# Kernel tuning notes

Hardware: AMD Instinct MI355X
Metric: run time of the kernel (lower is better)

## Reference

```python
import jax, jax.numpy as jnp
import numpy as np

N, E, IN, HID, OUT = 100000, 1600000, 128, 128, 64


def setup_inputs() -> dict:
    key = jax.random.key(0)
    ks = jax.random.split(key, 8)
    x = jax.random.normal(ks[0], (N, IN), dtype=jnp.float32)
    edge_index = jax.random.randint(ks[1], (2, E), 0, N, dtype=jnp.int64)
    s = lambda fan_in: 1.0 / np.sqrt(fan_in)
    W1_l = jax.random.normal(ks[2], (IN, HID), dtype=jnp.float32) * s(IN)
    W1_r = jax.random.normal(ks[3], (IN, HID), dtype=jnp.float32) * s(IN)
    b1 = jnp.zeros((HID,), dtype=jnp.float32)
    W2_l = jax.random.normal(ks[4], (HID, OUT), dtype=jnp.float32) * s(HID)
    W2_r = jax.random.normal(ks[5], (HID, OUT), dtype=jnp.float32) * s(HID)
    b2 = jnp.zeros((OUT,), dtype=jnp.float32)
    return {"x": x, "edge_index": edge_index, "W1_l": W1_l, "W1_r": W1_r,
            "b1": b1, "W2_l": W2_l, "W2_r": W2_r, "b2": b2}


def sage_conv(x, src, dst, W_l, W_r, b):
    """PyG SAGEConv (aggr='mean', root_weight=True): lin_l(mean_agg) + lin_r(x)."""
    n = x.shape[0]
    msg = x[src]                                              # [E, d] gather
    agg = jax.ops.segment_sum(msg, dst, num_segments=n)       # [N, d] scatter-add
    deg = jax.ops.segment_sum(jnp.ones_like(dst, dtype=x.dtype), dst,
                              num_segments=n)                 # [N]
    mean = agg / jnp.maximum(deg, 1.0)[:, None]
    return mean @ W_l + x @ W_r + b


def reference(x, edge_index, W1_l, W1_r, b1, W2_l, W2_r, b2):
    src, dst = edge_index[0], edge_index[1]
    h = sage_conv(x, src, dst, W1_l, W1_r, b1)
    h = jax.nn.relu(h)
    # dropout(p=0.5) is identity in eval mode
    out = sage_conv(h, src, dst, W2_l, W2_r, b2)
    return out
```

## Files before the change

kernel.cpp:

```cpp
#include <hip/hip_runtime.h>

#define NN 100000
#define NE 1600000
#define PSHIFT 9
#define PSZ 512
#define NP ((NN + PSZ - 1) / PSZ)
#define BCHUNK 8192
#define NBIN ((NE + BCHUNK - 1) / BCHUNK)
#define SRCMASK 0x1FFFF
#define BUCKET 9216
#define GMTILES ((NN + 63) / 64)
#define GEMM_GB 512

typedef __attribute__((ext_vector_type(8))) short short8;
typedef __attribute__((ext_vector_type(4))) float f32x4;

__device__ __forceinline__ ushort f2bf(float f) {
    uint u = __float_as_uint(f);
    return (ushort)((u + 0x7FFFu + ((u >> 16) & 1u)) >> 16);
}
__device__ __forceinline__ float bflo(uint u) { return __uint_as_float(u << 16); }
__device__ __forceinline__ float bfhi(uint u) { return __uint_as_float(u & 0xffff0000u); }
__device__ __forceinline__ uint packbf(float a, float b) {
    return (uint)f2bf(a) | ((uint)f2bf(b) << 16);
}

__global__ __launch_bounds__(256) void k_prep(const float* __restrict__ W1l,
                                              const float* __restrict__ W1r,
                                              const float* __restrict__ W2l,
                                              const float* __restrict__ W2r,
                                              ushort* __restrict__ WbT1,
                                              ushort* __restrict__ WbT2,
                                              int* __restrict__ gcur)
{
    const int tid = threadIdx.x;
    if (blockIdx.x == 0) {
        if (tid < NP) gcur[tid] = tid * BUCKET;
        return;
    }
    int i = (blockIdx.x - 1) * 256 + tid;
    if (i < 256 * 128) {
        int c = i >> 7, k = i & 127;
        float v = (c < 128) ? W1l[k * 128 + c] : W1r[k * 128 + (c - 128)];
        WbT1[i] = f2bf(v);
    } else if (i < 256 * 128 + 128 * 128) {
        int j = i - 256 * 128;
        int c = j >> 7, k = j & 127;
        float v = (c < 64) ? W2l[k * 64 + c] : W2r[k * 64 + (c - 64)];
        WbT2[j] = f2bf(v);
    }
}

__global__ __launch_bounds__(256) void k_binning(const int* __restrict__ src,
                                                 const int* __restrict__ dst,
                                                 int* __restrict__ gcur,
                                                 uint* __restrict__ packed)
{
    __shared__ int cnt[256];
    __shared__ int base[256];
    const int tid = threadIdx.x;
    const long e0 = (long)blockIdx.x * BCHUNK;
    cnt[tid] = 0;
    __syncthreads();
    for (int i = tid; i < BCHUNK; i += 256) {
        long e = e0 + i;
        if (e < NE) atomicAdd(&cnt[dst[e] >> PSHIFT], 1);
    }
    __syncthreads();
    if (cnt[tid] > 0) base[tid] = atomicAdd(&gcur[tid], cnt[tid]);
    cnt[tid] = 0;
    __syncthreads();
    for (int i = tid; i < BCHUNK; i += 256) {
        long e = e0 + i;
        if (e < NE) {
            int d = dst[e], s = src[e];
            int p = d >> PSHIFT;
            int ofs = atomicAdd(&cnt[p], 1);
            packed[base[p] + ofs] = (uint)s | ((uint)(d & (PSZ - 1)) << 17);
        }
    }
}

__global__ __launch_bounds__(256) void k_pfill(const uint* __restrict__ packed,
                                               const int* __restrict__ gcur,
                                               int* __restrict__ rowptr,
                                               int* __restrict__ rowend,
                                               int* __restrict__ col)
{
    __shared__ int cnt[PSZ];
    __shared__ int cur[PSZ];
    __shared__ int tot[256];
    const int p   = blockIdx.x;
    const int tid = threadIdx.x;
    const int beg = p * BUCKET, end = gcur[p];
    cnt[tid] = 0; cnt[tid + 256] = 0;
    __syncthreads();
    for (int i = beg + tid; i < end; i += 256)
        atomicAdd(&cnt[packed[i] >> 17], 1);
    __syncthreads();
    int v0 = cnt[tid * 2], v1 = cnt[tid * 2 + 1];
    int s  = v0 + v1;
    tot[tid] = s;
    __syncthreads();
    for (int off = 1; off < 256; off <<= 1) {
        int t = (tid >= off) ? tot[tid - off] : 0;
        __syncthreads();
        tot[tid] += t;
        __syncthreads();
    }
    int ex = tot[tid] - s + beg;
    cur[tid * 2]     = ex;
    cur[tid * 2 + 1] = ex + v0;
    int n0 = p * PSZ;
    if (n0 + tid * 2 < NN) {
        rowptr[n0 + tid * 2] = ex;
        rowend[n0 + tid * 2] = ex + v0;
    }
    if (n0 + tid * 2 + 1 < NN) {
        rowptr[n0 + tid * 2 + 1] = ex + v0;
        rowend[n0 + tid * 2 + 1] = ex + v0 + v1;
    }
    __syncthreads();
    for (int i = beg + tid; i < end; i += 256) {
        uint v = packed[i];
        int pos = atomicAdd(&cur[v >> 17], 1);
        col[pos] = (int)(v & SRCMASK);
    }
}

template <bool AF32, int CB, bool YF32>
__global__ __launch_bounds__(512) void k_gemm(const void* __restrict__ Ap,
                                              const ushort* __restrict__ Bt,
                                              const float* __restrict__ bias,
                                              ushort* __restrict__ zb,
                                              void* __restrict__ yout)
{
    constexpr int ZW = CB * 64;
    __shared__ ushort As[2][64 * 128];

    const int tid  = threadIdx.x;
    const int wid  = tid >> 6, lane = tid & 63;
    const int lr   = lane & 15;
    const int lk   = (lane >> 4) << 3;

    short8 bfr[4][CB];
#pragma unroll
    for (int ks = 0; ks < 4; ++ks)
#pragma unroll
        for (int nf = 0; nf < CB; ++nf) {
            int colB = wid * (16 * CB) + nf * 16 + lr;
            bfr[ks][nf] = *reinterpret_cast<const short8*>(
                Bt + (size_t)colB * 128 + ks * 32 + lk);
        }

    const int p0 = tid * 16, p1 = p0 + 8192;
    const int r0 = p0 >> 8, r1 = p1 >> 8;
    const int d0 = p0 ^ ((r0 & 7) << 4);
    const int d1 = p1 ^ ((r1 & 7) << 4);
    const int e0 = (p0 & 255) >> 1;
    const int e1 = (p1 & 255) >> 1;

    const short8 zero8 = {0, 0, 0, 0, 0, 0, 0, 0};
    short8 sA0, sA1;

    auto loadA = [&](int gr, int eo) -> short8 {
        if (gr >= NN) return zero8;
        if (AF32) {
            const float* A = (const float*)Ap;
            float4 f0 = *reinterpret_cast<const float4*>(A + (size_t)gr * 128 + eo);
            float4 f1 = *reinterpret_cast<const float4*>(A + (size_t)gr * 128 + eo + 4);
            short8 v;
            v[0] = (short)f2bf(f0.x); v[1] = (short)f2bf(f0.y);
            v[2] = (short)f2bf(f0.z); v[3] = (short)f2bf(f0.w);
            v[4] = (short)f2bf(f1.x); v[5] = (short)f2bf(f1.y);
            v[6] = (short)f2bf(f1.z); v[7] = (short)f2bf(f1.w);
            return v;
        } else {
            const ushort* A = (const ushort*)Ap;
            return *reinterpret_cast<const short8*>(A + (size_t)gr * 128 + eo);
        }
    };

    int t = blockIdx.x;
    sA0 = loadA(t * 64 + r0, e0);
    sA1 = loadA(t * 64 + r1, e1);

    int cur = 0;
    for (; t < GMTILES; t += GEMM_GB) {
        char* wbase = reinterpret_cast<char*>(As[cur]);
        *reinterpret_cast<short8*>(wbase + d0) = sA0;
        *reinterpret_cast<short8*>(wbase + d1) = sA1;
        __syncthreads();

        int tn = t + GEMM_GB;
        if (tn < GMTILES) {
            sA0 = loadA(tn * 64 + r0, e0);
            sA1 = loadA(tn * 64 + r1, e1);
        }

        f32x4 acc[4][CB];
#pragma unroll
        for (int mi = 0; mi < 4; ++mi)
#pragma unroll
            for (int nf = 0; nf < CB; ++nf) acc[mi][nf] = f32x4{0.f, 0.f, 0.f, 0.f};

        const char* pA = reinterpret_cast<const char*>(As[cur]);
#pragma unroll
        for (int ks = 0; ks < 4; ++ks) {
            int k2 = (ks * 32 + lk) * 2;
            short8 a[4];
#pragma unroll
            for (int mi = 0; mi < 4; ++mi) {
                int r = mi * 16 + lr;
                int byte = (r * 256 + k2) ^ ((r & 7) << 4);
                a[mi] = *reinterpret_cast<const short8*>(pA + byte);
            }
#pragma unroll
            for (int mi = 0; mi < 4; ++mi)
#pragma unroll
                for (int nf = 0; nf < CB; ++nf)
                    acc[mi][nf] = __builtin_amdgcn_mfma_f32_16x16x32_bf16(
                        a[mi], bfr[ks][nf], acc[mi][nf], 0, 0, 0);
        }

#pragma unroll
        for (int mi = 0; mi < 4; ++mi) {
#pragma unroll
            for (int nf = 0; nf < CB; ++nf) {
                int colg = wid * (16 * CB) + nf * 16 + lr;
#pragma unroll
                for (int rr = 0; rr < 4; ++rr) {
                    int rowg = t * 64 + mi * 16 + ((lane >> 4) << 2) + rr;
                    if (rowg < NN) {
                        float v = acc[mi][nf][rr];
                        if (colg < ZW) {
                            zb[(size_t)rowg * ZW + colg] = f2bf(v);
                        } else {
                            int c2 = colg - ZW;
                            if (YF32) ((float*)yout)[(size_t)rowg * ZW + c2]  = v + bias[c2];
                            else      ((ushort*)yout)[(size_t)rowg * ZW + c2] = f2bf(v + bias[c2]);
                        }
                    }
                }
            }
        }
        cur ^= 1;
    }
}

__global__ __launch_bounds__(256) void k_gather1(const ushort* __restrict__ z1b,
                                                 const ushort* __restrict__ y1b,
                                                 const int* __restrict__ rowptr,
                                                 const int* __restrict__ rowend,
                                                 const int* __restrict__ col,
                                                 ushort* __restrict__ hb)
{
    const int w = threadIdx.x >> 6, lane = threadIdx.x & 63;
    const int n = blockIdx.x * 4 + w;
    if (n >= NN) return;
    const int half = lane >> 5, li = lane & 31;
    const int beg = rowptr[n], end = rowend[n];
    const uint2* zu = (const uint2*)z1b;
    float a0 = 0.f, a1 = 0.f, a2 = 0.f, a3 = 0.f;
    int e = beg;
    for (; e + 7 < end; e += 8) {
        int s0 = col[e     + half];
        int s1 = col[e + 2 + half];
        int s2 = col[e + 4 + half];
        int s3 = col[e + 6 + half];
        uint2 u0 = zu[(size_t)s0 * 32 + li];
        uint2 u1 = zu[(size_t)s1 * 32 + li];
        uint2 u2 = zu[(size_t)s2 * 32 + li];
        uint2 u3 = zu[(size_t)s3 * 32 + li];
        a0 += bflo(u0.x) + bflo(u1.x) + bflo(u2.x) + bflo(u3.x);
        a1 += bfhi(u0.x) + bfhi(u1.x) + bfhi(u2.x) + bfhi(u3.x);
        a2 += bflo(u0.y) + bflo(u1.y) + bflo(u2.y) + bflo(u3.y);
        a3 += bfhi(u0.y) + bfhi(u1.y) + bfhi(u2.y) + bfhi(u3.y);
    }
    for (; e + 1 < end; e += 2) {
        int s0 = col[e + half];
        uint2 u0 = zu[(size_t)s0 * 32 + li];
        a0 += bflo(u0.x); a1 += bfhi(u0.x);
        a2 += bflo(u0.y); a3 += bfhi(u0.y);
    }
    if (e < end && half == 0) {
        int s0 = col[e];
        uint2 u0 = zu[(size_t)s0 * 32 + li];
        a0 += bflo(u0.x); a1 += bfhi(u0.x);
        a2 += bflo(u0.y); a3 += bfhi(u0.y);
    }
    a0 += __shfl_xor(a0, 32); a1 += __shfl_xor(a1, 32);
    a2 += __shfl_xor(a2, 32); a3 += __shfl_xor(a3, 32);
    if (half == 0) {
        float inv = 1.0f / (float)max(end - beg, 1);
        uint2 uy = ((const uint2*)y1b)[(size_t)n * 32 + li];
        float h0 = fmaxf(a0 * inv + bflo(uy.x), 0.f);
        float h1 = fmaxf(a1 * inv + bfhi(uy.x), 0.f);
        float h2 = fmaxf(a2 * inv + bflo(uy.y), 0.f);
        float h3 = fmaxf(a3 * inv + bfhi(uy.y), 0.f);
        uint2 o;
        o.x = packbf(h0, h1);
        o.y = packbf(h2, h3);
        ((uint2*)hb)[(size_t)n * 32 + li] = o;
    }
}

__global__ __launch_bounds__(256) void k_gather2(const ushort* __restrict__ z2b,
                                                 const float* __restrict__ y2f,
                                                 const int* __restrict__ rowptr,
                                                 const int* __restrict__ rowend,
                                                 const int* __restrict__ col,
                                                 float* __restrict__ out)
{
    const int w = threadIdx.x >> 6, lane = threadIdx.x & 63;
    const int n = blockIdx.x * 4 + w;
    if (n >= NN) return;
    const int quar = lane >> 4, li = lane & 15;
    const int beg = rowptr[n], end = rowend[n];
    const uint2* zu = (const uint2*)z2b;
    float a0 = 0.f, a1 = 0.f, a2 = 0.f, a3 = 0.f;
    int e = beg;
    for (; e + 15 < end; e += 16) {
        int s0 = col[e      + quar];
        int s1 = col[e + 4  + quar];
        int s2 = col[e + 8  + quar];
        int s3 = col[e + 12 + quar];
        uint2 u0 = zu[(size_t)s0 * 16 + li];
        uint2 u1 = zu[(size_t)s1 * 16 + li];
        uint2 u2 = zu[(size_t)s2 * 16 + li];
        uint2 u3 = zu[(size_t)s3 * 16 + li];
        a0 += bflo(u0.x) + bflo(u1.x) + bflo(u2.x) + bflo(u3.x);
        a1 += bfhi(u0.x) + bfhi(u1.x) + bfhi(u2.x) + bfhi(u3.x);
        a2 += bflo(u0.y) + bflo(u1.y) + bflo(u2.y) + bflo(u3.y);
        a3 += bfhi(u0.y) + bfhi(u1.y) + bfhi(u2.y) + bfhi(u3.y);
    }
    for (; e + 3 < end; e += 4) {
        int s0 = col[e + quar];
        uint2 u0 = zu[(size_t)s0 * 16 + li];
        a0 += bflo(u0.x); a1 += bfhi(u0.x);
        a2 += bflo(u0.y); a3 += bfhi(u0.y);
    }
    int rem = end - e;
    if (quar < rem) {
        int s0 = col[e + quar];
        uint2 u0 = zu[(size_t)s0 * 16 + li];
        a0 += bflo(u0.x); a1 += bfhi(u0.x);
        a2 += bflo(u0.y); a3 += bfhi(u0.y);
    }
    a0 += __shfl_xor(a0, 16); a1 += __shfl_xor(a1, 16);
    a2 += __shfl_xor(a2, 16); a3 += __shfl_xor(a3, 16);
    a0 += __shfl_xor(a0, 32); a1 += __shfl_xor(a1, 32);
    a2 += __shfl_xor(a2, 32); a3 += __shfl_xor(a3, 32);
    if (quar == 0) {
        float inv = 1.0f / (float)max(end - beg, 1);
        float4 y = ((const float4*)y2f)[(size_t)n * 16 + li];
        float4 o;
        o.x = a0 * inv + y.x;
        o.y = a1 * inv + y.y;
        o.z = a2 * inv + y.z;
        o.w = a3 * inv + y.w;
        ((float4*)out)[(size_t)n * 16 + li] = o;
    }
}

extern "C" void kernel_launch(void* const* d_in, const int* in_sizes, int n_in,
                              void* d_out, int out_size, void* d_ws, size_t ws_size,
                              hipStream_t stream)
{
    const float* x   = (const float*)d_in[0];
    const int*   ei  = (const int*)d_in[1];
    const float* W1l = (const float*)d_in[2];
    const float* W1r = (const float*)d_in[3];
    const float* b1  = (const float*)d_in[4];
    const float* W2l = (const float*)d_in[5];
    const float* W2r = (const float*)d_in[6];
    const float* b2  = (const float*)d_in[7];
    float* out = (float*)d_out;

    const int* src = ei;
    const int* dst = ei + NE;

    int*  rowptr = (int*)d_ws;
    int*  rowend = rowptr + NN;
    int*  gcur   = rowend + NN;
    uint* packed = (uint*)(gcur + 256);
    int*  colA   = (int*)(packed + (size_t)NP * BUCKET);
    uintptr_t p = (uintptr_t)(colA + (size_t)NP * BUCKET);
    p = (p + 255) & ~(uintptr_t)255;
    ushort* WbT1 = (ushort*)p;  p += (size_t)256 * 128 * 2;
    ushort* WbT2 = (ushort*)p;  p += (size_t)128 * 128 * 2;
    p = (p + 255) & ~(uintptr_t)255;
    ushort* z1b = (ushort*)p;   p += (size_t)NN * 128 * 2;
    ushort* y1b = (ushort*)p;   p += (size_t)NN * 128 * 2;
    ushort* hb  = (ushort*)p;   p += (size_t)NN * 128 * 2;
    ushort* z2b = z1b;
    float*  y2f = (float*)y1b;

    k_prep<<<1 + (256 * 128 + 128 * 128 + 255) / 256, 256, 0, stream>>>(
        W1l, W1r, W2l, W2r, WbT1, WbT2, gcur);

    k_binning<<<NBIN, 256, 0, stream>>>(src, dst, gcur, packed);
    k_pfill<<<NP, 256, 0, stream>>>(packed, gcur, rowptr, rowend, colA);

    k_gemm<true, 2, false><<<GEMM_GB, 512, 0, stream>>>(x, WbT1, b1, z1b, y1b);
    k_gather1<<<(NN + 3) / 4, 256, 0, stream>>>(z1b, y1b, rowptr, rowend, colA, hb);

    k_gemm<false, 1, true><<<GEMM_GB, 512, 0, stream>>>(hb, WbT2, b2, z2b, y2f);
    k_gather2<<<(NN + 3) / 4, 256, 0, stream>>>(z2b, y2f, rowptr, rowend, colA, out);
}
```

Baseline: 240.0 us.

## Slice feature columns per XCC and gather slices via persistent work-stealing blocks

```diff
diff --git a/kernel.cpp b/kernel.cpp
--- a/kernel.cpp
+++ b/kernel.cpp
@@ -11,6 +11,8 @@
 #define BUCKET 9216
 #define GMTILES ((NN + 63) / 64)
 #define GEMM_GB 512
+#define NCHUNK 1563
+#define GGRID 2048
 
 typedef __attribute__((ext_vector_type(8))) short short8;
 typedef __attribute__((ext_vector_type(4))) float f32x4;
@@ -23,6 +25,9 @@
 __device__ __forceinline__ float bfhi(uint u) { return __uint_as_float(u & 0xffff0000u); }
 __device__ __forceinline__ uint packbf(float a, float b) {
     return (uint)f2bf(a) | ((uint)f2bf(b) << 16);
+}
+__device__ __forceinline__ int xcc_id() {
+    return (int)(__builtin_amdgcn_s_getreg((3u << 11) | 20u) & 7u);
 }
 
 __global__ __launch_bounds__(256) void k_prep(const float* __restrict__ W1l,
@@ -31,11 +36,14 @@
                                               const float* __restrict__ W2r,
                                               ushort* __restrict__ WbT1,
                                               ushort* __restrict__ WbT2,
-                                              int* __restrict__ gcur)
+                                              int* __restrict__ gcur,
+                                              int* __restrict__ cnt1,
+                                              int* __restrict__ cnt2)
 {
     const int tid = threadIdx.x;
     if (blockIdx.x == 0) {
         if (tid < NP) gcur[tid] = tid * BUCKET;
+        if (tid < 8) { cnt1[tid] = 0; cnt2[tid] = 0; }
         return;
     }
     int i = (blockIdx.x - 1) * 256 + tid;
@@ -128,7 +136,7 @@
     }
 }
 
-template <bool AF32, int CB, bool YF32>
+template <int AMODE, int CB, bool YF32>
 __global__ __launch_bounds__(512) void k_gemm(const void* __restrict__ Ap,
                                               const ushort* __restrict__ Bt,
                                               const float* __restrict__ bias,
@@ -165,7 +173,7 @@
 
     auto loadA = [&](int gr, int eo) -> short8 {
         if (gr >= NN) return zero8;
-        if (AF32) {
+        if (AMODE == 0) {
             const float* A = (const float*)Ap;
             float4 f0 = *reinterpret_cast<const float4*>(A + (size_t)gr * 128 + eo);
             float4 f1 = *reinterpret_cast<const float4*>(A + (size_t)gr * 128 + eo + 4);
@@ -177,7 +185,8 @@
             return v;
         } else {
             const ushort* A = (const ushort*)Ap;
-            return *reinterpret_cast<const short8*>(A + (size_t)gr * 128 + eo);
+            return *reinterpret_cast<const short8*>(
+                A + (size_t)(eo >> 4) * NN * 16 + (size_t)gr * 16 + (eo & 15));
         }
     };
 
@@ -234,11 +243,17 @@
                     if (rowg < NN) {
                         float v = acc[mi][nf][rr];
                         if (colg < ZW) {
-                            zb[(size_t)rowg * ZW + colg] = f2bf(v);
+                            if (CB == 2)
+                                zb[(size_t)(colg >> 4) * NN * 16 + (size_t)rowg * 16 + (colg & 15)] = f2bf(v);
+                            else
+                                zb[(size_t)(colg >> 3) * NN * 8 + (size_t)rowg * 8 + (colg & 7)] = f2bf(v);
                         } else {
                             int c2 = colg - ZW;
-                            if (YF32) ((float*)yout)[(size_t)rowg * ZW + c2]  = v + bias[c2];
-                            else      ((ushort*)yout)[(size_t)rowg * ZW + c2] = f2bf(v + bias[c2]);
+                            float vb = v + bias[c2];
+                            if (YF32)
+                                ((float*)yout)[(size_t)(c2 >> 3) * NN * 8 + (size_t)rowg * 8 + (c2 & 7)] = vb;
+                            else
+                                ((ushort*)yout)[(size_t)(c2 >> 4) * NN * 16 + (size_t)rowg * 16 + (c2 & 15)] = f2bf(vb);
                         }
                     }
                 }
@@ -248,118 +263,120 @@
     }
 }
 
-__global__ __launch_bounds__(256) void k_gather1(const ushort* __restrict__ z1b,
-                                                 const ushort* __restrict__ y1b,
+__global__ __launch_bounds__(256) void k_gather1(const ushort* __restrict__ z1s,
+                                                 const ushort* __restrict__ y1s,
                                                  const int* __restrict__ rowptr,
                                                  const int* __restrict__ rowend,
                                                  const int* __restrict__ col,
-                                                 ushort* __restrict__ hb)
-{
-    const int w = threadIdx.x >> 6, lane = threadIdx.x & 63;
-    const int n = blockIdx.x * 4 + w;
-    if (n >= NN) return;
-    const int half = lane >> 5, li = lane & 31;
-    const int beg = rowptr[n], end = rowend[n];
-    const uint2* zu = (const uint2*)z1b;
-    float a0 = 0.f, a1 = 0.f, a2 = 0.f, a3 = 0.f;
-    int e = beg;
-    for (; e + 7 < end; e += 8) {
-        int s0 = col[e     + half];
-        int s1 = col[e + 2 + half];
-        int s2 = col[e + 4 + half];
-        int s3 = col[e + 6 + half];
-        uint2 u0 = zu[(size_t)s0 * 32 + li];
-        uint2 u1 = zu[(size_t)s1 * 32 + li];
-        uint2 u2 = zu[(size_t)s2 * 32 + li];
-        uint2 u3 = zu[(size_t)s3 * 32 + li];
-        a0 += bflo(u0.x) + bflo(u1.x) + bflo(u2.x) + bflo(u3.x);
-        a1 += bfhi(u0.x) + bfhi(u1.x) + bfhi(u2.x) + bfhi(u3.x);
-        a2 += bflo(u0.y) + bflo(u1.y) + bflo(u2.y) + bflo(u3.y);
-        a3 += bfhi(u0.y) + bfhi(u1.y) + bfhi(u2.y) + bfhi(u3.y);
-    }
-    for (; e + 1 < end; e += 2) {
-        int s0 = col[e + half];
-        uint2 u0 = zu[(size_t)s0 * 32 + li];
-        a0 += bflo(u0.x); a1 += bfhi(u0.x);
-        a2 += bflo(u0.y); a3 += bfhi(u0.y);
-    }
-    if (e < end && half == 0) {
-        int s0 = col[e];
-        uint2 u0 = zu[(size_t)s0 * 32 + li];
-        a0 += bflo(u0.x); a1 += bfhi(u0.x);
-        a2 += bflo(u0.y); a3 += bfhi(u0.y);
-    }
-    a0 += __shfl_xor(a0, 32); a1 += __shfl_xor(a1, 32);
-    a2 += __shfl_xor(a2, 32); a3 += __shfl_xor(a3, 32);
-    if (half == 0) {
-        float inv = 1.0f / (float)max(end - beg, 1);
-        uint2 uy = ((const uint2*)y1b)[(size_t)n * 32 + li];
-        float h0 = fmaxf(a0 * inv + bflo(uy.x), 0.f);
-        float h1 = fmaxf(a1 * inv + bfhi(uy.x), 0.f);
-        float h2 = fmaxf(a2 * inv + bflo(uy.y), 0.f);
-        float h3 = fmaxf(a3 * inv + bfhi(uy.y), 0.f);
-        uint2 o;
-        o.x = packbf(h0, h1);
-        o.y = packbf(h2, h3);
-        ((uint2*)hb)[(size_t)n * 32 + li] = o;
-    }
-}
-
-__global__ __launch_bounds__(256) void k_gather2(const ushort* __restrict__ z2b,
-                                                 const float* __restrict__ y2f,
+                                                 int* __restrict__ cnt,
+                                                 ushort* __restrict__ hbs)
+{
+    __shared__ int sh_c;
+    const int tid  = threadIdx.x;
+    const int wid  = tid >> 6, lane = tid & 63;
+    const int slot = lane >> 3, off = lane & 7;
+    const int s0   = xcc_id();
+
+    for (int si = 0; si < 8; ++si) {
+        int s = (s0 + si) & 7;
+        const uint* zu = (const uint*)z1s + (size_t)s * NN * 8;
+        const uint* yu = (const uint*)y1s + (size_t)s * NN * 8;
+        uint*       hu = (uint*)hbs       + (size_t)s * NN * 8;
+        while (true) {
+            __syncthreads();
+            if (tid == 0) sh_c = atomicAdd(&cnt[s], 1);
+            __syncthreads();
+            int c = sh_c;
+            if (c >= NCHUNK) break;
+            int nb = c * 64 + wid * 16;
+            for (int j = 0; j < 16; ++j) {
+                int n = nb + j;
+                if (n >= NN) break;
+                int beg = rowptr[n], end = rowend[n];
+                float a0 = 0.f, a1 = 0.f;
+                int e = beg + slot;
+                for (; e + 8 < end; e += 16) {
+                    int c0 = col[e], c1 = col[e + 8];
+                    uint u0 = zu[(size_t)c0 * 8 + off];
+                    uint u1 = zu[(size_t)c1 * 8 + off];
+                    a0 += bflo(u0) + bflo(u1);
+                    a1 += bfhi(u0) + bfhi(u1);
+                }
+                if (e < end) {
+                    uint u0 = zu[(size_t)col[e] * 8 + off];
+                    a0 += bflo(u0); a1 += bfhi(u0);
+                }
+                a0 += __shfl_xor(a0, 8);  a1 += __shfl_xor(a1, 8);
+                a0 += __shfl_xor(a0, 16); a1 += __shfl_xor(a1, 16);
+                a0 += __shfl_xor(a0, 32); a1 += __shfl_xor(a1, 32);
+                if (slot == 0) {
+                    float inv = 1.f / (float)max(end - beg, 1);
+                    uint uy = yu[(size_t)n * 8 + off];
+                    float h0 = fmaxf(a0 * inv + bflo(uy), 0.f);
+                    float h1 = fmaxf(a1 * inv + bfhi(uy), 0.f);
+                    hu[(size_t)n * 8 + off] = packbf(h0, h1);
+                }
+            }
+        }
+    }
+}
+
+__global__ __launch_bounds__(256) void k_gather2(const ushort* __restrict__ z2s,
+                                                 const float* __restrict__ y2s,
                                                  const int* __restrict__ rowptr,
                                                  const int* __restrict__ rowend,
                                                  const int* __restrict__ col,
+                                                 int* __restrict__ cnt,
                                                  float* __restrict__ out)
 {
-    const int w = threadIdx.x >> 6, lane = threadIdx.x & 63;
-    const int n = blockIdx.x * 4 + w;
-    if (n >= NN) return;
-    const int quar = lane >> 4, li = lane & 15;
-    const int beg = rowptr[n], end = rowend[n];
-    const uint2* zu = (const uint2*)z2b;
-    float a0 = 0.f, a1 = 0.f, a2 = 0.f, a3 = 0.f;
-    int e = beg;
-    for (; e + 15 < end; e += 16) {
-        int s0 = col[e      + quar];
-        int s1 = col[e + 4  + quar];
-        int s2 = col[e + 8  + quar];
-        int s3 = col[e + 12 + quar];
-        uint2 u0 = zu[(size_t)s0 * 16 + li];
-        uint2 u1 = zu[(size_t)s1 * 16 + li];
-        uint2 u2 = zu[(size_t)s2 * 16 + li];
-        uint2 u3 = zu[(size_t)s3 * 16 + li];
-        a0 += bflo(u0.x) + bflo(u1.x) + bflo(u2.x) + bflo(u3.x);
-        a1 += bfhi(u0.x) + bfhi(u1.x) + bfhi(u2.x) + bfhi(u3.x);
-        a2 += bflo(u0.y) + bflo(u1.y) + bflo(u2.y) + bflo(u3.y);
-        a3 += bfhi(u0.y) + bfhi(u1.y) + bfhi(u2.y) + bfhi(u3.y);
-    }
-    for (; e + 3 < end; e += 4) {
-        int s0 = col[e + quar];
-        uint2 u0 = zu[(size_t)s0 * 16 + li];
-        a0 += bflo(u0.x); a1 += bfhi(u0.x);
-        a2 += bflo(u0.y); a3 += bfhi(u0.y);
-    }
-    int rem = end - e;
-    if (quar < rem) {
-        int s0 = col[e + quar];
-        uint2 u0 = zu[(size_t)s0 * 16 + li];
-        a0 += bflo(u0.x); a1 += bfhi(u0.x);
-        a2 += bflo(u0.y); a3 += bfhi(u0.y);
-    }
-    a0 += __shfl_xor(a0, 16); a1 += __shfl_xor(a1, 16);
-    a2 += __shfl_xor(a2, 16); a3 += __shfl_xor(a3, 16);
-    a0 += __shfl_xor(a0, 32); a1 += __shfl_xor(a1, 32);
-    a2 += __shfl_xor(a2, 32); a3 += __shfl_xor(a3, 32);
-    if (quar == 0) {
-        float inv = 1.0f / (float)max(end - beg, 1);
-        float4 y = ((const float4*)y2f)[(size_t)n * 16 + li];
-        float4 o;
-        o.x = a0 * inv + y.x;
-        o.y = a1 * inv + y.y;
-        o.z = a2 * inv + y.z;
-        o.w = a3 * inv + y.w;
-        ((float4*)out)[(size_t)n * 16 + li] = o;
+    __shared__ int sh_c;
+    const int tid  = threadIdx.x;
+    const int wid  = tid >> 6, lane = tid & 63;
+    const int slot = lane >> 2, off = lane & 3;
+    const int s0   = xcc_id();
+
+    for (int si = 0; si < 8; ++si) {
+        int s = (s0 + si) & 7;
+        const uint*   zu = (const uint*)z2s   + (size_t)s * NN * 4;
+        const float2* yu = (const float2*)y2s + (size_t)s * NN * 4;
+        while (true) {
+            __syncthreads();
+            if (tid == 0) sh_c = atomicAdd(&cnt[s], 1);
+            __syncthreads();
+            int c = sh_c;
+            if (c >= NCHUNK) break;
+            int nb = c * 64 + wid * 16;
+            for (int j = 0; j < 16; ++j) {
+                int n = nb + j;
+                if (n >= NN) break;
+                int beg = rowptr[n], end = rowend[n];
+                float a0 = 0.f, a1 = 0.f;
+                int e = beg + slot;
+                for (; e + 16 < end; e += 32) {
+                    int c0 = col[e], c1 = col[e + 16];
+                    uint u0 = zu[(size_t)c0 * 4 + off];
+                    uint u1 = zu[(size_t)c1 * 4 + off];
+                    a0 += bflo(u0) + bflo(u1);
+                    a1 += bfhi(u0) + bfhi(u1);
+                }
+                if (e < end) {
+                    uint u0 = zu[(size_t)col[e] * 4 + off];
+                    a0 += bflo(u0); a1 += bfhi(u0);
+                }
+                a0 += __shfl_xor(a0, 4);  a1 += __shfl_xor(a1, 4);
+                a0 += __shfl_xor(a0, 8);  a1 += __shfl_xor(a1, 8);
+                a0 += __shfl_xor(a0, 16); a1 += __shfl_xor(a1, 16);
+                a0 += __shfl_xor(a0, 32); a1 += __shfl_xor(a1, 32);
+                if (slot == 0) {
+                    float inv = 1.f / (float)max(end - beg, 1);
+                    float2 y = yu[(size_t)n * 4 + off];
+                    float2 o;
+                    o.x = a0 * inv + y.x;
+                    o.y = a1 * inv + y.y;
+                    ((float2*)out)[(size_t)n * 32 + s * 4 + off] = o;
+                }
+            }
+        }
     }
 }
 
@@ -383,6 +400,8 @@
     int*  rowptr = (int*)d_ws;
     int*  rowend = rowptr + NN;
     int*  gcur   = rowend + NN;
+    int*  cnt1   = gcur + 200;
+    int*  cnt2   = gcur + 216;
     uint* packed = (uint*)(gcur + 256);
     int*  colA   = (int*)(packed + (size_t)NP * BUCKET);
     uintptr_t p = (uintptr_t)(colA + (size_t)NP * BUCKET);
@@ -390,21 +409,21 @@
     ushort* WbT1 = (ushort*)p;  p += (size_t)256 * 128 * 2;
     ushort* WbT2 = (ushort*)p;  p += (size_t)128 * 128 * 2;
     p = (p + 255) & ~(uintptr_t)255;
-    ushort* z1b = (ushort*)p;   p += (size_t)NN * 128 * 2;
-    ushort* y1b = (ushort*)p;   p += (size_t)NN * 128 * 2;
-    ushort* hb  = (ushort*)p;   p += (size_t)NN * 128 * 2;
-    ushort* z2b = z1b;
-    float*  y2f = (float*)y1b;
+    ushort* z1s = (ushort*)p;   p += (size_t)NN * 128 * 2;
+    ushort* y1s = (ushort*)p;   p += (size_t)NN * 128 * 2;
+    ushort* hbs = (ushort*)p;   p += (size_t)NN * 128 * 2;
+    ushort* z2s = z1s;
+    float*  y2s = (float*)y1s;
 
     k_prep<<<1 + (256 * 128 + 128 * 128 + 255) / 256, 256, 0, stream>>>(
-        W1l, W1r, W2l, W2r, WbT1, WbT2, gcur);
+        W1l, W1r, W2l, W2r, WbT1, WbT2, gcur, cnt1, cnt2);
 
     k_binning<<<NBIN, 256, 0, stream>>>(src, dst, gcur, packed);
     k_pfill<<<NP, 256, 0, stream>>>(packed, gcur, rowptr, rowend, colA);
 
-    k_gemm<true, 2, false><<<GEMM_GB, 512, 0, stream>>>(x, WbT1, b1, z1b, y1b);
-    k_gather1<<<(NN + 3) / 4, 256, 0, stream>>>(z1b, y1b, rowptr, rowend, colA, hb);
-
-    k_gemm<false, 1, true><<<GEMM_GB, 512, 0, stream>>>(hb, WbT2, b2, z2b, y2f);
-    k_gather2<<<(NN + 3) / 4, 256, 0, stream>>>(z2b, y2f, rowptr, rowend, colA, out);
-}
+    k_gemm<0, 2, false><<<GEMM_GB, 512, 0, stream>>>(x, WbT1, b1, z1s, y1s);
+    k_gather1<<<GGRID, 256, 0, stream>>>(z1s, y1s, rowptr, rowend, colA, cnt1, hbs);
+
+    k_gemm<1, 1, true><<<GEMM_GB, 512, 0, stream>>>(hbs, WbT2, b2, z2s, y2s);
+    k_gather2<<<GGRID, 256, 0, stream>>>(z2s, y2s, rowptr, rowend, colA, cnt2, out);
+}
```

Result: slower. 906.0 us (+277.5%).
